# Kernel optimization log

Hardware: AMD Instinct MI355X
Metric: run time of the kernel (lower is better)

Reference implementation:

```python
import jax, jax.numpy as jnp
import numpy as np

TOP_K = 8  # config['n_experts_per_token']


def setup_inputs() -> dict:
    key = jax.random.key(0)
    k1, k2 = jax.random.split(key)
    d_hidden, n_experts, n_tokens = 4096, 64, 32768
    x = jax.random.normal(k1, (n_tokens, d_hidden), dtype=jnp.float32)
    # nn.Linear weight, shape [num_experts, d_hidden], kaiming-ish scale
    W_g = jax.random.normal(k2, (n_experts, d_hidden), dtype=jnp.float32) / np.sqrt(d_hidden)
    return {"x": x, "W_g": W_g}


def reference(x, W_g):
    # logits = x @ W_g^T : [n_tokens, n_experts]
    logits = jnp.einsum('td,ed->te', x, W_g)
    scores = jax.nn.softmax(logits, axis=-1)
    # torch.topk(sorted=False) returns the same value/index set; lax.top_k is sorted
    vals, idx = jax.lax.top_k(scores, TOP_K)
    return vals, idx
```

## Files before the change

### kernel.cpp

```cpp
#include <hip/hip_runtime.h>
#include <hip/hip_fp16.h>


typedef _Float16 half8 __attribute__((ext_vector_type(8)));
typedef float floatx4 __attribute__((ext_vector_type(4)));

constexpr int D = 4096;
constexpr int NE = 64;
constexpr int MBLK = 64;
constexpr int BK = 64;
constexpr int KCHUNKS = D / BK;

__device__ __forceinline__ void split8(float4 p, float4 q, float sc, half8& h, half8& l) {
    float f[8] = {p.x, p.y, p.z, p.w, q.x, q.y, q.z, q.w};
#pragma unroll
    for (int i = 0; i < 8; ++i) {
        float v = f[i] * sc;
        _Float16 hi = (_Float16)v;
        h[i] = hi;
        l[i] = (_Float16)(v - (float)hi);
    }
}

__global__ __launch_bounds__(256, 2) void moe_gate_kernel(
    const float* __restrict__ x, const float* __restrict__ wg,
    float* __restrict__ out_vals, float* __restrict__ out_idx,
    int* __restrict__ flag_ws, int cap)
{
    __shared__ alignas(16) _Float16 Xh[MBLK * BK];
    __shared__ alignas(16) _Float16 Xl[MBLK * BK];
    __shared__ alignas(16) _Float16 Wh[NE * BK];
    __shared__ alignas(16) _Float16 Wl[NE * BK];

    const int tid  = (int)threadIdx.x;
    const int lane = tid & 63;
    const int wv   = tid >> 6;
    const int tb   = (int)blockIdx.x * MBLK;

    const int s0 = tid, s1 = tid + 256;
    const int t0 = s0 >> 3, k80 = s0 & 7;
    const int t1 = s1 >> 3, k81 = s1 & 7;

    const float* xp0 = x  + (size_t)(tb + t0) * D + k80 * 8;
    const float* xp1 = x  + (size_t)(tb + t1) * D + k81 * 8;
    const float* wp0 = wg + (size_t)t0 * D + k80 * 8;
    const float* wp1 = wg + (size_t)t1 * D + k81 * 8;

    const int xo0 = (((t0 >> 4) * 2 + (k80 >> 2)) * 64 + (k80 & 3) * 16 + (t0 & 15)) * 8;
    const int xo1 = (((t1 >> 4) * 2 + (k81 >> 2)) * 64 + (k81 & 3) * 16 + (t1 & 15)) * 8;

    float4 ra0, ra1, rb0, rb1, rc0, rc1, rd0, rd1;
#define LOADCHUNK(kc) do { const int off_ = (kc) * BK;                        \
        ra0 = *(const float4*)(xp0 + off_); ra1 = *(const float4*)(xp0 + off_ + 4); \
        rb0 = *(const float4*)(xp1 + off_); rb1 = *(const float4*)(xp1 + off_ + 4); \
        rc0 = *(const float4*)(wp0 + off_); rc1 = *(const float4*)(wp0 + off_ + 4); \
        rd0 = *(const float4*)(wp1 + off_); rd1 = *(const float4*)(wp1 + off_ + 4); } while (0)

    floatx4 acc[4] = {{0,0,0,0},{0,0,0,0},{0,0,0,0},{0,0,0,0}};

    LOADCHUNK(0);
    for (int kc = 0; kc < KCHUNKS; ++kc) {
        half8 hx0, lx0, hx1, lx1, hw0, lw0, hw1, lw1;
        split8(ra0, ra1, 1.0f,  hx0, lx0);
        split8(rb0, rb1, 1.0f,  hx1, lx1);
        split8(rc0, rc1, 64.0f, hw0, lw0);
        split8(rd0, rd1, 64.0f, hw1, lw1);
        if (kc) __syncthreads();
        *(half8*)(Xh + xo0) = hx0; *(half8*)(Xl + xo0) = lx0;
        *(half8*)(Xh + xo1) = hx1; *(half8*)(Xl + xo1) = lx1;
        *(half8*)(Wh + xo0) = hw0; *(half8*)(Wl + xo0) = lw0;
        *(half8*)(Wh + xo1) = hw1; *(half8*)(Wl + xo1) = lw1;
        if (kc + 1 < KCHUNKS) LOADCHUNK(kc + 1);
        __syncthreads();
#pragma unroll
        for (int ks = 0; ks < 2; ++ks) {
            const half8 ah = *(const half8*)(Xh + ((wv * 2 + ks) * 64 + lane) * 8);
            const half8 al = *(const half8*)(Xl + ((wv * 2 + ks) * 64 + lane) * 8);
#pragma unroll
            for (int nt = 0; nt < 4; ++nt) {
                const half8 bh = *(const half8*)(Wh + ((nt * 2 + ks) * 64 + lane) * 8);
                const half8 bl = *(const half8*)(Wl + ((nt * 2 + ks) * 64 + lane) * 8);
                acc[nt] = __builtin_amdgcn_mfma_f32_16x16x32_f16(ah, bh, acc[nt], 0, 0, 0);
                acc[nt] = __builtin_amdgcn_mfma_f32_16x16x32_f16(al, bh, acc[nt], 0, 0, 0);
                acc[nt] = __builtin_amdgcn_mfma_f32_16x16x32_f16(ah, bl, acc[nt], 0, 0, 0);
            }
        }
    }
#undef LOADCHUNK

    const int g = lane >> 4, c = lane & 15;
    const float inv64 = 0.015625f;
#pragma unroll
    for (int r = 0; r < 4; ++r) {
        float s[4];
#pragma unroll
        for (int nt = 0; nt < 4; ++nt) s[nt] = acc[nt][r] * inv64;
        float m = fmaxf(fmaxf(s[0], s[1]), fmaxf(s[2], s[3]));
#pragma unroll
        for (int off = 1; off < 16; off <<= 1) m = fmaxf(m, __shfl_xor(m, off));
        float p[4]; float t = 0.0f;
#pragma unroll
        for (int nt = 0; nt < 4; ++nt) { p[nt] = expf(s[nt] - m); t += p[nt]; }
#pragma unroll
        for (int off = 1; off < 16; off <<= 1) t += __shfl_xor(t, off);
        const float inv = 1.0f / t;
#pragma unroll
        for (int nt = 0; nt < 4; ++nt) p[nt] *= inv;

        const int tok = tb + wv * 16 + g * 4 + r;
        float prev = 0.0f;
        bool flagged = false;
#pragma unroll
        for (int i = 0; i < 9; ++i) {
            float bv = p[0]; int bn = 0;
            if (p[1] > bv) { bv = p[1]; bn = 1; }
            if (p[2] > bv) { bv = p[2]; bn = 2; }
            if (p[3] > bv) { bv = p[3]; bn = 3; }
            int be = bn * 16 + c;
#pragma unroll
            for (int off = 1; off < 16; off <<= 1) {
                float ov = __shfl_xor(bv, off);
                int   oe = __shfl_xor(be, off);
                if (ov > bv || (ov == bv && oe < be)) { bv = ov; be = oe; }
            }
            if (i > 0 && (prev - bv) < prev * 5e-5f) flagged = true;
            prev = bv;
            if (i < 8 && c == i) {
                out_vals[(size_t)tok * 8 + i] = bv;
                out_idx [(size_t)tok * 8 + i] = (float)be;
            }
            if (c == (be & 15)) p[be >> 4] = -1.0f;
        }
        if (flagged && c == 0 && cap > 0) {
            int pos = atomicAdd(flag_ws, 1);
            if (pos < cap) flag_ws[4 + pos] = tok;
        }
    }
}

__global__ __launch_bounds__(256) void moe_refine_kernel(
    const float* __restrict__ x, const float* __restrict__ wg,
    float* __restrict__ out_vals, float* __restrict__ out_idx,
    const int* __restrict__ flag_ws, int cap)
{
    const int count = min(flag_ws[0], cap);
    const int* list = flag_ws + 4;
    __shared__ double part[256];
    for (int it = (int)blockIdx.x; it < count; it += (int)gridDim.x) {
        const int tok = list[it];
        const int e = (int)threadIdx.x & 63, ch = (int)threadIdx.x >> 6;
        const float4* xr = (const float4*)(x + (size_t)tok * D + ch * 1024);
        const float4* wr = (const float4*)(wg + (size_t)e * D + ch * 1024);
        double s0 = 0, s1 = 0, s2 = 0, s3 = 0;
#pragma unroll 4
        for (int k = 0; k < 256; ++k) {
            float4 a = xr[k], b = wr[k];
            s0 += (double)a.x * (double)b.x; s1 += (double)a.y * (double)b.y;
            s2 += (double)a.z * (double)b.z; s3 += (double)a.w * (double)b.w;
        }
        part[threadIdx.x] = (s0 + s1) + (s2 + s3);
        __syncthreads();
        if (threadIdx.x < 64) {
            double l = part[e] + part[e + 64] + part[e + 128] + part[e + 192];
            double m = l;
#pragma unroll
            for (int off = 1; off < 64; off <<= 1) m = fmax(m, __shfl_xor(m, off));
            double p = exp(l - m), Z = p;
#pragma unroll
            for (int off = 1; off < 64; off <<= 1) Z += __shfl_xor(Z, off);
            double key = l;
            for (int i = 0; i < 8; ++i) {
                double bk = key; int bi = e; double bp = p;
#pragma unroll
                for (int off = 1; off < 64; off <<= 1) {
                    double ok = __shfl_xor(bk, off);
                    int    oi = __shfl_xor(bi, off);
                    double op = __shfl_xor(bp, off);
                    if (ok > bk || (ok == bk && oi < bi)) { bk = ok; bi = oi; bp = op; }
                }
                if (e == i) {
                    out_vals[(size_t)tok * 8 + i] = (float)(bp / Z);
                    out_idx [(size_t)tok * 8 + i] = (float)bi;
                }
                if (e == bi) key = -1.0e300;
            }
        }
        __syncthreads();
    }
}

extern "C" void kernel_launch(void* const* d_in, const int* in_sizes, int n_in,
                              void* d_out, int out_size, void* d_ws, size_t ws_size,
                              hipStream_t stream) {
    const float* x  = (const float*)d_in[0];
    const float* wg = (const float*)d_in[1];
    const int n_tokens = in_sizes[0] / D;
    float* out_vals = (float*)d_out;
    float* out_idx  = out_vals + (size_t)n_tokens * 8;
    int cap = 0;
    if (ws_size > 32) {
        size_t c = (ws_size - 32) / sizeof(int);
        cap = (int)(c > 32768 ? 32768 : c);
    }
    hipMemsetAsync(d_ws, 0, 16, stream);
    const int grid = n_tokens / MBLK;
    hipLaunchKernelGGL(moe_gate_kernel, dim3(grid), dim3(256), 0, stream,
                       x, wg, out_vals, out_idx, (int*)d_ws, cap);
    hipLaunchKernelGGL(moe_refine_kernel, dim3(256), dim3(256), 0, stream,
                       x, wg, out_vals, out_idx, (const int*)d_ws, cap);
}
```

Before: 795.4 us.

## Pre-split gate weights into fp16 hi/lo in workspace, double-buffer X tiles

A new pre-pass kernel converts W_g once into fp16 high/low parts in MFMA fragment order inside the workspace. The gate kernel then reads B fragments straight from global/L2 rather than re-splitting and staging W through LDS in every block. X staging is double-buffered in LDS, which allows one barrier per K-chunk and overlaps the next load with compute. The risks are extra global traffic for W fragments per block, a fixed workspace-size assumption (about 2 MB), and an extra launch.

```diff
diff --git a/kernel.cpp b/kernel.cpp
--- a/kernel.cpp
+++ b/kernel.cpp
@@ -11,82 +11,105 @@
 constexpr int BK = 64;
 constexpr int KCHUNKS = D / BK;
 
-__device__ __forceinline__ void split8(float4 p, float4 q, float sc, half8& h, half8& l) {
-    float f[8] = {p.x, p.y, p.z, p.w, q.x, q.y, q.z, q.w};
+constexpr size_t WS_WH_OFF = (size_t)1 << 20;
+constexpr size_t WS_WL_OFF = ((size_t)1 << 20) + ((size_t)512 << 10);
+
+__device__ __forceinline__ void split16(const float4& a, const float4& b,
+                                        const float4& c, const float4& d, float sc,
+                                        half8& h0, half8& h1, half8& l0, half8& l1) {
+    float f[16] = {a.x,a.y,a.z,a.w,b.x,b.y,b.z,b.w,c.x,c.y,c.z,c.w,d.x,d.y,d.z,d.w};
+#pragma unroll
+    for (int i = 0; i < 16; ++i) {
+        float v = f[i] * sc;
+        _Float16 hi = (_Float16)v;
+        _Float16 lo = (_Float16)(v - (float)hi);
+        if (i < 8) { h0[i] = hi; l0[i] = lo; }
+        else       { h1[i - 8] = hi; l1[i - 8] = lo; }
+    }
+}
+
+__global__ __launch_bounds__(256) void presplit_w_kernel(
+    const float* __restrict__ wg, _Float16* __restrict__ wh, _Float16* __restrict__ wl)
+{
+    const int gid = (int)blockIdx.x * 256 + (int)threadIdx.x;
+    const int e = gid >> 9, k8 = gid & 511;
+    const float4* src = (const float4*)(wg + (size_t)e * D + k8 * 8);
+    float4 a = src[0], b = src[1];
+    float f[8] = {a.x,a.y,a.z,a.w,b.x,b.y,b.z,b.w};
+    half8 h, l;
 #pragma unroll
     for (int i = 0; i < 8; ++i) {
-        float v = f[i] * sc;
+        float v = f[i] * 64.0f;
         _Float16 hi = (_Float16)v;
         h[i] = hi;
         l[i] = (_Float16)(v - (float)hi);
     }
+    const int k = k8 * 8, kc = k >> 6, ks = (k >> 5) & 1, kk = k & 31;
+    const int lane = (e & 15) | ((kk >> 3) << 4);
+    const int nt = e >> 4;
+    const size_t off = ((((size_t)kc * 4 + nt) * 2 + ks) * 64 + lane) * 8;
+    *(half8*)(wh + off) = h;
+    *(half8*)(wl + off) = l;
 }
 
 __global__ __launch_bounds__(256, 2) void moe_gate_kernel(
-    const float* __restrict__ x, const float* __restrict__ wg,
+    const float* __restrict__ x,
+    const _Float16* __restrict__ whp, const _Float16* __restrict__ wlp,
     float* __restrict__ out_vals, float* __restrict__ out_idx,
     int* __restrict__ flag_ws, int cap)
 {
-    __shared__ alignas(16) _Float16 Xh[MBLK * BK];
-    __shared__ alignas(16) _Float16 Xl[MBLK * BK];
-    __shared__ alignas(16) _Float16 Wh[NE * BK];
-    __shared__ alignas(16) _Float16 Wl[NE * BK];
+    __shared__ alignas(16) _Float16 Xh[2][MBLK * BK];
+    __shared__ alignas(16) _Float16 Xl[2][MBLK * BK];
 
     const int tid  = (int)threadIdx.x;
     const int lane = tid & 63;
     const int wv   = tid >> 6;
     const int tb   = (int)blockIdx.x * MBLK;
 
-    const int s0 = tid, s1 = tid + 256;
-    const int t0 = s0 >> 3, k80 = s0 & 7;
-    const int t1 = s1 >> 3, k81 = s1 & 7;
-
-    const float* xp0 = x  + (size_t)(tb + t0) * D + k80 * 8;
-    const float* xp1 = x  + (size_t)(tb + t1) * D + k81 * 8;
-    const float* wp0 = wg + (size_t)t0 * D + k80 * 8;
-    const float* wp1 = wg + (size_t)t1 * D + k81 * 8;
-
-    const int xo0 = (((t0 >> 4) * 2 + (k80 >> 2)) * 64 + (k80 & 3) * 16 + (t0 & 15)) * 8;
-    const int xo1 = (((t1 >> 4) * 2 + (k81 >> 2)) * 64 + (k81 & 3) * 16 + (t1 & 15)) * 8;
-
-    float4 ra0, ra1, rb0, rb1, rc0, rc1, rd0, rd1;
-#define LOADCHUNK(kc) do { const int off_ = (kc) * BK;                        \
-        ra0 = *(const float4*)(xp0 + off_); ra1 = *(const float4*)(xp0 + off_ + 4); \
-        rb0 = *(const float4*)(xp1 + off_); rb1 = *(const float4*)(xp1 + off_ + 4); \
-        rc0 = *(const float4*)(wp0 + off_); rc1 = *(const float4*)(wp0 + off_ + 4); \
-        rd0 = *(const float4*)(wp1 + off_); rd1 = *(const float4*)(wp1 + off_ + 4); } while (0)
+    const int row = tid >> 2, kg = tid & 3;
+    const int m = row & 15, mt = row >> 4;
+    const float* xp = x + (size_t)(tb + row) * D + kg * 16;
+    const int off0 = ((mt * 2 + (kg >> 1)) * 64 + m + (kg & 1) * 32) * 8;
+
+    float4 r0, r1, r2, r3;
+#define LOADX(kc) do { const float4* p_ = (const float4*)(xp + (size_t)(kc) * BK); \
+        r0 = p_[0]; r1 = p_[1]; r2 = p_[2]; r3 = p_[3]; } while (0)
+#define STAGEX(nb) do { half8 h0_, h1_, l0_, l1_;                          \
+        split16(r0, r1, r2, r3, 1.0f, h0_, h1_, l0_, l1_);                 \
+        *(half8*)&Xh[nb][off0]       = h0_; *(half8*)&Xh[nb][off0 + 128] = h1_; \
+        *(half8*)&Xl[nb][off0]       = l0_; *(half8*)&Xl[nb][off0 + 128] = l1_; } while (0)
 
     floatx4 acc[4] = {{0,0,0,0},{0,0,0,0},{0,0,0,0},{0,0,0,0}};
 
-    LOADCHUNK(0);
+    LOADX(0);
+    STAGEX(0);
+    __syncthreads();
+    LOADX(1);
+
     for (int kc = 0; kc < KCHUNKS; ++kc) {
-        half8 hx0, lx0, hx1, lx1, hw0, lw0, hw1, lw1;
-        split8(ra0, ra1, 1.0f,  hx0, lx0);
-        split8(rb0, rb1, 1.0f,  hx1, lx1);
-        split8(rc0, rc1, 64.0f, hw0, lw0);
-        split8(rd0, rd1, 64.0f, hw1, lw1);
-        if (kc) __syncthreads();
-        *(half8*)(Xh + xo0) = hx0; *(half8*)(Xl + xo0) = lx0;
-        *(half8*)(Xh + xo1) = hx1; *(half8*)(Xl + xo1) = lx1;
-        *(half8*)(Wh + xo0) = hw0; *(half8*)(Wl + xo0) = lw0;
-        *(half8*)(Wh + xo1) = hw1; *(half8*)(Wl + xo1) = lw1;
-        if (kc + 1 < KCHUNKS) LOADCHUNK(kc + 1);
-        __syncthreads();
+        const int cur = kc & 1;
 #pragma unroll
         for (int ks = 0; ks < 2; ++ks) {
-            const half8 ah = *(const half8*)(Xh + ((wv * 2 + ks) * 64 + lane) * 8);
-            const half8 al = *(const half8*)(Xl + ((wv * 2 + ks) * 64 + lane) * 8);
+            const half8 ah = *(const half8*)&Xh[cur][((wv * 2 + ks) * 64 + lane) * 8];
+            const half8 al = *(const half8*)&Xl[cur][((wv * 2 + ks) * 64 + lane) * 8];
 #pragma unroll
             for (int nt = 0; nt < 4; ++nt) {
-                const half8 bh = *(const half8*)(Wh + ((nt * 2 + ks) * 64 + lane) * 8);
-                const half8 bl = *(const half8*)(Wl + ((nt * 2 + ks) * 64 + lane) * 8);
+                const size_t bo = ((((size_t)kc * 4 + nt) * 2 + ks) * 64 + lane) * 8;
+                const half8 bh = *(const half8*)(whp + bo);
+                const half8 bl = *(const half8*)(wlp + bo);
                 acc[nt] = __builtin_amdgcn_mfma_f32_16x16x32_f16(ah, bh, acc[nt], 0, 0, 0);
                 acc[nt] = __builtin_amdgcn_mfma_f32_16x16x32_f16(al, bh, acc[nt], 0, 0, 0);
                 acc[nt] = __builtin_amdgcn_mfma_f32_16x16x32_f16(ah, bl, acc[nt], 0, 0, 0);
             }
         }
-    }
-#undef LOADCHUNK
+        if (kc + 1 < KCHUNKS) {
+            STAGEX(cur ^ 1);
+            __syncthreads();
+            if (kc + 2 < KCHUNKS) LOADX(kc + 2);
+        }
+    }
+#undef LOADX
+#undef STAGEX
 
     const int g = lane >> 4, c = lane & 15;
     const float inv64 = 0.015625f;
@@ -95,12 +118,12 @@
         float s[4];
 #pragma unroll
         for (int nt = 0; nt < 4; ++nt) s[nt] = acc[nt][r] * inv64;
-        float m = fmaxf(fmaxf(s[0], s[1]), fmaxf(s[2], s[3]));
-#pragma unroll
-        for (int off = 1; off < 16; off <<= 1) m = fmaxf(m, __shfl_xor(m, off));
+        float mx = fmaxf(fmaxf(s[0], s[1]), fmaxf(s[2], s[3]));
+#pragma unroll
+        for (int off = 1; off < 16; off <<= 1) mx = fmaxf(mx, __shfl_xor(mx, off));
         float p[4]; float t = 0.0f;
 #pragma unroll
-        for (int nt = 0; nt < 4; ++nt) { p[nt] = expf(s[nt] - m); t += p[nt]; }
+        for (int nt = 0; nt < 4; ++nt) { p[nt] = expf(s[nt] - mx); t += p[nt]; }
 #pragma unroll
         for (int off = 1; off < 16; off <<= 1) t += __shfl_xor(t, off);
         const float inv = 1.0f / t;
@@ -197,15 +220,16 @@
     const int n_tokens = in_sizes[0] / D;
     float* out_vals = (float*)d_out;
     float* out_idx  = out_vals + (size_t)n_tokens * 8;
-    int cap = 0;
-    if (ws_size > 32) {
-        size_t c = (ws_size - 32) / sizeof(int);
-        cap = (int)(c > 32768 ? 32768 : c);
-    }
+    _Float16* wh = (_Float16*)((char*)d_ws + WS_WH_OFF);
+    _Float16* wl = (_Float16*)((char*)d_ws + WS_WL_OFF);
+    int cap = n_tokens;
+    if ((size_t)(16 + cap * 4) > WS_WH_OFF) cap = (int)((WS_WH_OFF - 16) / 4);
+
     hipMemsetAsync(d_ws, 0, 16, stream);
-    const int grid = n_tokens / MBLK;
-    hipLaunchKernelGGL(moe_gate_kernel, dim3(grid), dim3(256), 0, stream,
-                       x, wg, out_vals, out_idx, (int*)d_ws, cap);
+    hipLaunchKernelGGL(presplit_w_kernel, dim3(NE * (D / 8) / 256), dim3(256), 0, stream,
+                       wg, wh, wl);
+    hipLaunchKernelGGL(moe_gate_kernel, dim3(n_tokens / MBLK), dim3(256), 0, stream,
+                       x, wh, wl, out_vals, out_idx, (int*)d_ws, cap);
     hipLaunchKernelGGL(moe_refine_kernel, dim3(256), dim3(256), 0, stream,
                        x, wg, out_vals, out_idx, (const int*)d_ws, cap);
 }
```

Result: slower. 913.3 us (+14.8%).
